# Optimization experiments

Measured on AMD Instinct MI355X. Metric: run time of the kernel, lower is better.

## Reference

```python
import jax, jax.numpy as jnp
import numpy as np

N = 50000          # nodes
E = 400000         # edges
F = 128            # num_embeddings
NUM_TYPES = 100    # num_atoms (embedding vocab)
CUTOFF = 5.0
N_RBF = 20


def _silu(x):
    return x * jax.nn.sigmoid(x)


def setup_inputs() -> dict:
    key = jax.random.key(0)
    ks = jax.random.split(key, 16)
    pos = jax.random.normal(ks[0], (N, 3), dtype=jnp.float32) * 3.0
    z = jax.random.randint(ks[1], (N,), 0, NUM_TYPES)
    dst = jax.random.randint(ks[2], (E,), 0, N)
    # ensure src != dst so distances are nonzero
    src = (dst + 1 + jax.random.randint(ks[3], (E,), 0, N - 1)) % N
    def lin(k, fan_in, fan_out):
        kw, kb = jax.random.split(k)
        lim = 1.0 / np.sqrt(fan_in)
        W = jax.random.uniform(kw, (fan_out, fan_in), minval=-lim, maxval=lim, dtype=jnp.float32)
        b = jax.random.uniform(kb, (fan_out,), minval=-lim, maxval=lim, dtype=jnp.float32)
        return W, b
    emb_table = jax.random.normal(ks[4], (NUM_TYPES, F), dtype=jnp.float32)
    Wp1, bp1 = lin(ks[5], F, F)
    Wp2, bp2 = lin(ks[6], F, 3 * F)
    Ww, bw = lin(ks[7], N_RBF, 3 * F)
    Wu, bu = lin(ks[8], F, F)
    Wv, bv = lin(ks[9], F, F)
    Wu1, bu1 = lin(ks[10], 2 * F, F)
    Wu2, bu2 = lin(ks[11], F, 3 * F)
    return dict(pos=pos, emb_table=emb_table,
                Wp1=Wp1, bp1=bp1, Wp2=Wp2, bp2=bp2, Ww=Ww, bw=bw,
                Wu=Wu, bu=bu, Wv=Wv, bv=bv, Wu1=Wu1, bu1=bu1, Wu2=Wu2, bu2=bu2,
                z=z, src=src, dst=dst)


def painn_forward(pos, emb_table, Wp1, bp1, Wp2, bp2, Ww, bw, Wu, bu, Wv, bv,
                  Wu1, bu1, Wu2, bu2, z, src, dst):
    s = emb_table[z]                                  # [N,F] scalar features
    v = jnp.zeros((N, F, 3), dtype=s.dtype)          # equivariant features

    # ---- message block ----
    phi = _silu(s @ Wp1.T + bp1) @ Wp2.T + bp2       # [N,3F]
    rel = pos[dst] - pos[src]                        # [E,3]
    d = jnp.maximum(jnp.linalg.norm(rel, axis=-1), 1e-9)  # [E]
    n = jnp.arange(1, N_RBF + 1, dtype=jnp.float32)
    rbf = jnp.sin(n * jnp.pi * d[:, None] / CUTOFF) / d[:, None]   # [E,20]
    Wf = rbf @ Ww.T + bw                             # [E,3F]
    split = phi[src] * Wf                            # [E,3F] gated message
    ds = jax.ops.segment_sum(split[:, :F], dst, num_segments=N)    # [N,F]
    direction = rel / d[:, None]                     # [E,3]
    dv_e = v[src] * split[:, F:2 * F, None] + split[:, 2 * F:, None] * direction[:, None, :]  # [E,F,3]
    dv = jax.ops.segment_sum(dv_e, dst, num_segments=N)            # [N,F,3]
    s = s + ds
    v = v + dv

    # ---- update block ----
    U = jnp.einsum('nfc,gf->ngc', v, Wu) + bu[:, None]   # [N,F,3]
    V = jnp.einsum('nfc,gf->ngc', v, Wv) + bv[:, None]   # [N,F,3]
    Vn = jnp.linalg.norm(V, axis=-1)                     # [N,F]
    h = jnp.concatenate([s, Vn], axis=-1)                # [N,2F]
    a = _silu(h @ Wu1.T + bu1) @ Wu2.T + bu2             # [N,3F]
    dv2 = U * a[:, :F, None]                             # [N,F,3]
    ds2 = a[:, F:2 * F] + jnp.sum(U * V, axis=-1) * a[:, 2 * F:]   # [N,F]
    return s + ds2, v + dv2


def reference(pos, emb_table, Wp1, bp1, Wp2, bp2, Ww, bw, Wu, bu, Wv, bv,
              Wu1, bu1, Wu2, bu2, z, src, dst):
    return painn_forward(pos, emb_table, Wp1, bp1, Wp2, bp2, Ww, bw, Wu, bu,
                         Wv, bv, Wu1, bu1, Wu2, bu2, z, src, dst)
```

## Files before the change

### kernel.cpp

```cpp
#include <hip/hip_runtime.h>

#define NN 50000
#define EE 400000
#define FF 128
#define NRBF 20
#define MAXDEG 64
#define PI_OVER_CUT 0.6283185307179586f

typedef _Float16 h8 __attribute__((ext_vector_type(8)));
typedef float    f4 __attribute__((ext_vector_type(4)));

union pk32 { unsigned int u; _Float16 h[2]; };

__global__ __launch_bounds__(256) void k_bucket(const int* __restrict__ dst,
                                                int* __restrict__ counts,
                                                int* __restrict__ slots) {
    int e = blockIdx.x * 256 + threadIdx.x;
    if (e < EE) {
        int n = dst[e];
        int slot = atomicAdd(&counts[n], 1);
        if (slot < MAXDEG) slots[n * MAXDEG + slot] = e;
    }
}

__global__ __launch_bounds__(256) void k_wconv(
    const float* __restrict__ Wu, const float* __restrict__ Wv,
    const float* __restrict__ Wu1, const float* __restrict__ Wu2,
    const float* __restrict__ Wp1, const float* __restrict__ Wp2,
    const float* __restrict__ Ww, const float* __restrict__ bw,
    _Float16* __restrict__ Wuh, _Float16* __restrict__ Wvh,
    _Float16* __restrict__ Wu1h, _Float16* __restrict__ Wu2h,
    _Float16* __restrict__ Wp1h, _Float16* __restrict__ Wp2h,
    _Float16* __restrict__ Wwh32, int* __restrict__ counts)
{
    int i = blockIdx.x * 256 + threadIdx.x;
    if (i < NN) counts[i] = 0;
    if (i < 16384) { Wuh[i] = (_Float16)Wu[i]; Wvh[i] = (_Float16)Wv[i];
                     Wp1h[i] = (_Float16)Wp1[i]; }
    if (i < 32768) { Wu1h[i] = (_Float16)Wu1[i]; }
    if (i < 49152) { Wu2h[i] = (_Float16)Wu2[i]; Wp2h[i] = (_Float16)Wp2[i]; }
    if (i < 8192) {
        int col = i >> 5, k = i & 31;
        int sr = col < 128 ? col : col + 128;
        _Float16 v = (_Float16)0.f;
        if (k < 20)       v = (_Float16)Ww[sr * NRBF + k];
        else if (k == 20) v = (_Float16)bw[sr];
        Wwh32[i] = v;
    }
}

__global__ __launch_bounds__(256) void k_node_phi_mfma(
    const float* __restrict__ emb, const int* __restrict__ z,
    const _Float16* __restrict__ Wp1h, const float* __restrict__ bp1,
    const _Float16* __restrict__ Wp2h, const float* __restrict__ bp2,
    unsigned int* __restrict__ phi_pk, _Float16* __restrict__ s_h)
{
    __shared__ _Float16 Ss[32 * 128];
    __shared__ _Float16 H1s[32 * 128];

    const int t    = threadIdx.x;
    const int lane = t & 63;
    const int w    = t >> 6;
    const int lr   = lane & 15;
    const int lq   = lane >> 4;
    const int n0   = blockIdx.x * 32;
    const f4 z4 = {0.f, 0.f, 0.f, 0.f};

    for (int i = t; i < 512; i += 256) {
        int n = i >> 4, gr = i & 15;
        int nn = n0 + n; if (nn > NN - 1) nn = NN - 1;
        const float* sp = &emb[(size_t)z[nn] * FF + gr * 8];
        float4 aa = *(const float4*)sp;
        float4 bb = *(const float4*)(sp + 4);
        h8 hv;
        hv[0] = (_Float16)aa.x; hv[1] = (_Float16)aa.y;
        hv[2] = (_Float16)aa.z; hv[3] = (_Float16)aa.w;
        hv[4] = (_Float16)bb.x; hv[5] = (_Float16)bb.y;
        hv[6] = (_Float16)bb.z; hv[7] = (_Float16)bb.w;
        *(h8*)&Ss[(n * 16 + (gr ^ (n & 15))) * 8] = hv;
        *(h8*)&s_h[(size_t)nn * FF + gr * 8] = hv;
    }
    __syncthreads();

    f4 acc1[2][2];
    #pragma unroll
    for (int a = 0; a < 2; ++a)
        #pragma unroll
        for (int m = 0; m < 2; ++m) acc1[a][m] = z4;
    {
        const _Float16* bb = Wp1h + (size_t)lr * 128 + lq * 8;
        #pragma unroll
        for (int g2 = 0; g2 < 2; ++g2) {
            h8 bf[4];
            #pragma unroll
            for (int ks = 0; ks < 4; ++ks)
                bf[ks] = *(const h8*)(bb + ((2 * w + g2) * 16) * 128 + ks * 32);
            #pragma unroll
            for (int mt = 0; mt < 2; ++mt) {
                const int r = mt * 16 + lr;
                #pragma unroll
                for (int ks = 0; ks < 4; ++ks) {
                    h8 af = *(const h8*)&Ss[(r * 16 + ((ks * 4 + lq) ^ (r & 15))) * 8];
                    acc1[g2][mt] = __builtin_amdgcn_mfma_f32_16x16x32_f16(
                        af, bf[ks], acc1[g2][mt], 0, 0, 0);
                }
            }
        }
    }
    #pragma unroll
    for (int g2 = 0; g2 < 2; ++g2) {
        const int g = (2 * w + g2) * 16 + lr;
        const float b1 = bp1[g];
        #pragma unroll
        for (int mt = 0; mt < 2; ++mt)
            #pragma unroll
            for (int r = 0; r < 4; ++r) {
                float x = acc1[g2][mt][r] + b1;
                float y = x / (1.f + __expf(-x));
                int n = mt * 16 + lq * 4 + r;
                H1s[(n * 16 + ((g >> 3) ^ (n & 15))) * 8 + (g & 7)] = (_Float16)y;
            }
    }
    __syncthreads();

    f4 accS[2][2], accV[2][2];
    #pragma unroll
    for (int a = 0; a < 2; ++a)
        #pragma unroll
        for (int m = 0; m < 2; ++m) { accS[a][m] = z4; accV[a][m] = z4; }
    {
        const _Float16* bbs = Wp2h + (size_t)lr * 128 + lq * 8;
        const _Float16* bbv = Wp2h + (size_t)(256 + lr) * 128 + lq * 8;
        #pragma unroll
        for (int g2 = 0; g2 < 2; ++g2) {
            h8 bfs[4], bfv[4];
            #pragma unroll
            for (int ks = 0; ks < 4; ++ks) {
                bfs[ks] = *(const h8*)(bbs + ((2 * w + g2) * 16) * 128 + ks * 32);
                bfv[ks] = *(const h8*)(bbv + ((2 * w + g2) * 16) * 128 + ks * 32);
            }
            #pragma unroll
            for (int mt = 0; mt < 2; ++mt) {
                const int r = mt * 16 + lr;
                #pragma unroll
                for (int ks = 0; ks < 4; ++ks) {
                    h8 af = *(const h8*)&H1s[(r * 16 + ((ks * 4 + lq) ^ (r & 15))) * 8];
                    accS[g2][mt] = __builtin_amdgcn_mfma_f32_16x16x32_f16(
                        af, bfs[ks], accS[g2][mt], 0, 0, 0);
                    accV[g2][mt] = __builtin_amdgcn_mfma_f32_16x16x32_f16(
                        af, bfv[ks], accV[g2][mt], 0, 0, 0);
                }
            }
        }
    }
    #pragma unroll
    for (int g2 = 0; g2 < 2; ++g2) {
        const int g = (2 * w + g2) * 16 + lr;
        const float bsa = bp2[g], bva = bp2[256 + g];
        #pragma unroll
        for (int mt = 0; mt < 2; ++mt)
            #pragma unroll
            for (int r = 0; r < 4; ++r) {
                int n = mt * 16 + lq * 4 + r;
                int nn = n0 + n;
                if (nn < NN) {
                    pk32 pk;
                    pk.h[0] = (_Float16)(accS[g2][mt][r] + bsa);
                    pk.h[1] = (_Float16)(accV[g2][mt][r] + bva);
                    phi_pk[(size_t)nn * FF + g] = pk.u;
                }
            }
    }
}

__global__ __launch_bounds__(128) void k_edge_mfma(
    const float* __restrict__ pos,
    const _Float16* __restrict__ Wwh32,
    const int* __restrict__ src,
    const int* __restrict__ counts, const int* __restrict__ slots,
    const unsigned int* __restrict__ phi_pk,
    _Float16* __restrict__ s_h,
    _Float16* __restrict__ xg)
{
    __shared__ _Float16 A[16 * 32];
    __shared__ float dirs[16][4];
    __shared__ unsigned int wf[16 * 130];

    const int t    = threadIdx.x;
    const int lane = t & 63;
    const int w    = t >> 6;
    const int lr   = lane & 15;
    const int lq   = lane >> 4;
    const int n    = blockIdx.x;
    const int m    = t & 15;
    const int kk   = t >> 4;
    const f4 z4 = {0.f, 0.f, 0.f, 0.f};

    h8 bf[8];
    #pragma unroll
    for (int j = 0; j < 8; ++j)
        bf[j] = *(const h8*)&Wwh32[(size_t)((w * 8 + j) * 16 + lr) * 32 + lq * 8];

    const float px = pos[3 * n], py = pos[3 * n + 1], pz = pos[3 * n + 2];

    int deg = counts[n];
    deg = deg > MAXDEG ? MAXDEG : deg;

    const size_t gi = (size_t)n * FF + t;
    float s_old = (float)s_h[gi];

    float acc_s = 0.f, av0 = 0.f, av1 = 0.f, av2 = 0.f;

    for (int t0 = 0; t0 < deg; t0 += 16) {
        const int degT = (deg - t0) < 16 ? (deg - t0) : 16;
        __syncthreads();
        {
            int mc = (m < degT) ? m : 0;
            int e  = slots[n * MAXDEG + t0 + mc];
            int sI = src[e];
            float rx = px - pos[3 * sI];
            float ry = py - pos[3 * sI + 1];
            float rz = pz - pos[3 * sI + 2];
            float d = sqrtf(rx * rx + ry * ry + rz * rz);
            d = fmaxf(d, 1e-9f);
            float di = 1.f / d;
            if (t < 16) {
                dirs[t][0] = rx * di;
                dirs[t][1] = ry * di;
                dirs[t][2] = rz * di;
                dirs[t][3] = __int_as_float(sI);
            }
            float v0 = __sinf((float)(kk + 1) * PI_OVER_CUT * d) * di;
            float v1 = __sinf((float)(kk + 9) * PI_OVER_CUT * d) * di;
            float v2;
            if (kk < 4)       v2 = __sinf((float)(kk + 17) * PI_OVER_CUT * d) * di;
            else if (kk == 4) v2 = 1.0f;
            else              v2 = 0.f;
            #define STO(K, V) A[m * 32 + (((K) >> 3) ^ (m & 3)) * 8 + ((K) & 7)] = (_Float16)(V)
            STO(kk,      v0);
            STO(kk + 8,  v1);
            STO(kk + 16, v2);
            STO(kk + 24, 0.f);
            #undef STO
        }
        __syncthreads();
        {
            h8 af = *(const h8*)&A[(lr * 4 + (lq ^ (lr & 3))) * 8];
            #pragma unroll
            for (int j = 0; j < 8; ++j) {
                f4 dd = __builtin_amdgcn_mfma_f32_16x16x32_f16(af, bf[j], z4, 0, 0, 0);
                #pragma unroll
                for (int r = 0; r < 4; ++r) {
                    int mm = lq * 4 + r;
                    ((_Float16*)&wf[mm * 130 + j * 16 + lr])[w] = (_Float16)dd[r];
                }
            }
        }
        __syncthreads();
        {
            unsigned int phr[16];
            #pragma unroll
            for (int mm = 0; mm < 16; ++mm) {
                int sim = __float_as_int(dirs[mm][3]);
                phr[mm] = (mm < degT) ? phi_pk[(size_t)sim * FF + t] : 0u;
            }
            #pragma unroll
            for (int mm = 0; mm < 16; ++mm) {
                if (mm < degT) {
                    pk32 ph, wfu;
                    ph.u  = phr[mm];
                    wfu.u = wf[mm * 130 + t];
                    float ps = (float)ph.h[0] * (float)wfu.h[0];
                    float pv = (float)ph.h[1] * (float)wfu.h[1];
                    acc_s += ps;
                    av0 = fmaf(pv, dirs[mm][0], av0);
                    av1 = fmaf(pv, dirs[mm][1], av1);
                    av2 = fmaf(pv, dirs[mm][2], av2);
                }
            }
        }
    }

    s_h[gi] = (_Float16)(s_old + acc_s);
    xg[((size_t)n * 3 + 0) * FF + t] = (_Float16)av0;
    xg[((size_t)n * 3 + 1) * FF + t] = (_Float16)av1;
    xg[((size_t)n * 3 + 2) * FF + t] = (_Float16)av2;
}

__global__ __launch_bounds__(256) void k_update_mfma(
    const _Float16* __restrict__ xg, const _Float16* __restrict__ s_h,
    const _Float16* __restrict__ Wuh, const _Float16* __restrict__ Wvh,
    const _Float16* __restrict__ Wu1h, const _Float16* __restrict__ Wu2h,
    const float* __restrict__ bu, const float* __restrict__ bv,
    const float* __restrict__ bu1, const float* __restrict__ bu2,
    float* __restrict__ s_io, float* __restrict__ v_io)
{
    __shared__ _Float16 Xs[48 * 128];
    __shared__ _Float16 Hs[16 * 256];
    __shared__ _Float16 H1s[16 * 128];

    const int t    = threadIdx.x;
    const int lane = t & 63;
    const int w    = t >> 6;
    const int lr   = lane & 15;
    const int lq   = lane >> 4;
    const int n0   = blockIdx.x * 16;
    const f4 z4 = {0.f, 0.f, 0.f, 0.f};

    for (int i = t; i < 768; i += 256) {
        int row = i >> 4, gr = i & 15;
        int n = row & 15, c = row >> 4;
        int nn = n0 + n; if (nn > NN - 1) nn = NN - 1;
        uint4 d = *(const uint4*)&xg[((size_t)nn * 3 + c) * FF + gr * 8];
        *(uint4*)&Xs[(row * 16 + (gr ^ n)) * 8] = d;
    }
    {
        int n = t >> 4, gr = t & 15;
        int nn = n0 + n; if (nn > NN - 1) nn = NN - 1;
        uint4 d = *(const uint4*)&s_h[(size_t)nn * FF + gr * 8];
        *(uint4*)&Hs[(n * 32 + (gr ^ n)) * 8] = d;
    }
    __syncthreads();

    f4 accU[2][3], accV[2][3];
    #pragma unroll
    for (int a = 0; a < 2; ++a)
        #pragma unroll
        for (int c = 0; c < 3; ++c) { accU[a][c] = z4; accV[a][c] = z4; }

    {
        const _Float16* bb = Wuh + (size_t)lr * 128 + lq * 8;
        h8 bfr[2][4];
        #pragma unroll
        for (int g2 = 0; g2 < 2; ++g2)
            #pragma unroll
            for (int ks = 0; ks < 4; ++ks)
                bfr[g2][ks] = *(const h8*)(bb + ((2 * w + g2) * 16) * 128 + ks * 32);
        #pragma unroll
        for (int c = 0; c < 3; ++c) {
            const int rr = c * 16 + lr;
            h8 af[4];
            #pragma unroll
            for (int ks = 0; ks < 4; ++ks)
                af[ks] = *(const h8*)&Xs[(rr * 16 + ((ks * 4 + lq) ^ lr)) * 8];
            #pragma unroll
            for (int g2 = 0; g2 < 2; ++g2)
                #pragma unroll
                for (int ks = 0; ks < 4; ++ks)
                    accU[g2][c] = __builtin_amdgcn_mfma_f32_16x16x32_f16(
                        af[ks], bfr[g2][ks], accU[g2][c], 0, 0, 0);
        }
    }
    {
        const _Float16* bb = Wvh + (size_t)lr * 128 + lq * 8;
        h8 bfr[2][4];
        #pragma unroll
        for (int g2 = 0; g2 < 2; ++g2)
            #pragma unroll
            for (int ks = 0; ks < 4; ++ks)
                bfr[g2][ks] = *(const h8*)(bb + ((2 * w + g2) * 16) * 128 + ks * 32);
        #pragma unroll
        for (int c = 0; c < 3; ++c) {
            const int rr = c * 16 + lr;
            h8 af[4];
            #pragma unroll
            for (int ks = 0; ks < 4; ++ks)
                af[ks] = *(const h8*)&Xs[(rr * 16 + ((ks * 4 + lq) ^ lr)) * 8];
            #pragma unroll
            for (int g2 = 0; g2 < 2; ++g2)
                #pragma unroll
                for (int ks = 0; ks < 4; ++ks)
                    accV[g2][c] = __builtin_amdgcn_mfma_f32_16x16x32_f16(
                        af[ks], bfr[g2][ks], accV[g2][c], 0, 0, 0);
        }
    }

    float uvr[2][4];
    #pragma unroll
    for (int g2 = 0; g2 < 2; ++g2) {
        const int g = (2 * w + g2) * 16 + lr;
        const float bU = bu[g], bV = bv[g];
        #pragma unroll
        for (int r = 0; r < 4; ++r) {
            float Ux = accU[g2][0][r] + bU;
            float Uy = accU[g2][1][r] + bU;
            float Uz = accU[g2][2][r] + bU;
            float Vx = accV[g2][0][r] + bV;
            float Vy = accV[g2][1][r] + bV;
            float Vz = accV[g2][2][r] + bV;
            accU[g2][0][r] = Ux;
            accU[g2][1][r] = Uy;
            accU[g2][2][r] = Uz;
            uvr[g2][r] = Ux * Vx + Uy * Vy + Uz * Vz;
            float vn = sqrtf(Vx * Vx + Vy * Vy + Vz * Vz);
            int n = lq * 4 + r;
            int gr = 16 + (g >> 3);
            Hs[(n * 32 + (gr ^ n)) * 8 + (g & 7)] = (_Float16)vn;
        }
    }
    __syncthreads();

    f4 acc2[2];
    acc2[0] = z4; acc2[1] = z4;
    {
        const _Float16* bb = Wu1h + (size_t)lr * 256 + lq * 8;
        #pragma unroll
        for (int g2 = 0; g2 < 2; ++g2) {
            h8 bfr[8];
            #pragma unroll
            for (int ks = 0; ks < 8; ++ks)
                bfr[ks] = *(const h8*)(bb + ((2 * w + g2) * 16) * 256 + ks * 32);
            #pragma unroll
            for (int ks = 0; ks < 8; ++ks) {
                h8 af = *(const h8*)&Hs[(lr * 32 + ((ks * 4 + lq) ^ lr)) * 8];
                acc2[g2] = __builtin_amdgcn_mfma_f32_16x16x32_f16(
                    af, bfr[ks], acc2[g2], 0, 0, 0);
            }
        }
    }
    #pragma unroll
    for (int g2 = 0; g2 < 2; ++g2) {
        const int g = (2 * w + g2) * 16 + lr;
        const float b1 = bu1[g];
        #pragma unroll
        for (int r = 0; r < 4; ++r) {
            float x = acc2[g2][r] + b1;
            float y = x / (1.f + __expf(-x));
            int n = lq * 4 + r;
            H1s[(n * 16 + ((g >> 3) ^ n)) * 8 + (g & 7)] = (_Float16)y;
        }
    }
    __syncthreads();

    f4 acc3[3][2];
    #pragma unroll
    for (int a = 0; a < 3; ++a) { acc3[a][0] = z4; acc3[a][1] = z4; }
    {
        const _Float16* bb = Wu2h + (size_t)lr * 128 + lq * 8;
        #pragma unroll
        for (int ai = 0; ai < 3; ++ai)
            #pragma unroll
            for (int g2 = 0; g2 < 2; ++g2) {
                const int jt = ai * 8 + 2 * w + g2;
                h8 bfr[4];
                #pragma unroll
                for (int ks = 0; ks < 4; ++ks)
                    bfr[ks] = *(const h8*)(bb + (size_t)(jt * 16) * 128 + ks * 32);
                #pragma unroll
                for (int ks = 0; ks < 4; ++ks) {
                    h8 af = *(const h8*)&H1s[(lr * 16 + ((ks * 4 + lq) ^ lr)) * 8];
                    acc3[ai][g2] = __builtin_amdgcn_mfma_f32_16x16x32_f16(
                        af, bfr[ks], acc3[ai][g2], 0, 0, 0);
                }
            }
    }

    #pragma unroll
    for (int g2 = 0; g2 < 2; ++g2) {
        const int g = (2 * w + g2) * 16 + lr;
        const float b1 = bu2[g], b2 = bu2[128 + g], b3 = bu2[256 + g];
        #pragma unroll
        for (int r = 0; r < 4; ++r) {
            int n = lq * 4 + r;
            int nn = n0 + n;
            if (nn < NN) {
                float a1 = acc3[0][g2][r] + b1;
                float a2 = acc3[1][g2][r] + b2;
                float a3 = acc3[2][g2][r] + b3;
                size_t gi = (size_t)nn * FF + g;
                float s1 = (float)Hs[(n * 32 + ((g >> 3) ^ n)) * 8 + (g & 7)];
                s_io[gi] = s1 + a2 + uvr[g2][r] * a3;
                float vx = (float)Xs[((0 * 16 + n) * 16 + ((g >> 3) ^ n)) * 8 + (g & 7)];
                float vy = (float)Xs[((1 * 16 + n) * 16 + ((g >> 3) ^ n)) * 8 + (g & 7)];
                float vz = (float)Xs[((2 * 16 + n) * 16 + ((g >> 3) ^ n)) * 8 + (g & 7)];
                v_io[gi * 3 + 0] = vx + accU[g2][0][r] * a1;
                v_io[gi * 3 + 1] = vy + accU[g2][1][r] * a1;
                v_io[gi * 3 + 2] = vz + accU[g2][2][r] * a1;
            }
        }
    }
}

extern "C" void kernel_launch(void* const* d_in, const int* in_sizes, int n_in,
                              void* d_out, int out_size, void* d_ws, size_t ws_size,
                              hipStream_t stream)
{
    const float* pos = (const float*)d_in[0];
    const float* emb = (const float*)d_in[1];
    const float* Wp1 = (const float*)d_in[2];
    const float* bp1 = (const float*)d_in[3];
    const float* Wp2 = (const float*)d_in[4];
    const float* bp2 = (const float*)d_in[5];
    const float* Ww  = (const float*)d_in[6];
    const float* bw  = (const float*)d_in[7];
    const float* Wu  = (const float*)d_in[8];
    const float* bu  = (const float*)d_in[9];
    const float* Wv  = (const float*)d_in[10];
    const float* bv  = (const float*)d_in[11];
    const float* Wu1 = (const float*)d_in[12];
    const float* bu1 = (const float*)d_in[13];
    const float* Wu2 = (const float*)d_in[14];
    const float* bu2 = (const float*)d_in[15];
    const int* z   = (const int*)d_in[16];
    const int* src = (const int*)d_in[17];
    const int* dst = (const int*)d_in[18];

    float* s_io = (float*)d_out;
    float* v_io = (float*)d_out + (size_t)NN * FF;

    char* ws = (char*)d_ws;
    unsigned int* phi_pk = (unsigned int*)ws;
    _Float16* xg    = (_Float16*)(phi_pk + (size_t)NN * FF);
    _Float16* s_h   = xg + (size_t)NN * 3 * FF;
    _Float16* Wuh   = s_h + (size_t)NN * FF;
    _Float16* Wvh   = Wuh  + 128 * 128;
    _Float16* Wu1h  = Wvh  + 128 * 128;
    _Float16* Wu2h  = Wu1h + 128 * 256;
    _Float16* Wp1h  = Wu2h + 384 * 128;
    _Float16* Wp2h  = Wp1h + 128 * 128;
    _Float16* Wwh32 = Wp2h + 384 * 128;
    int* counts = (int*)(Wwh32 + 256 * 32);
    int* slots  = counts + NN;

    k_wconv <<<196, 256, 0, stream>>>(Wu, Wv, Wu1, Wu2, Wp1, Wp2, Ww, bw,
                                      Wuh, Wvh, Wu1h, Wu2h, Wp1h, Wp2h, Wwh32,
                                      counts);
    k_bucket<<<(EE + 255) / 256, 256, 0, stream>>>(dst, counts, slots);
    k_node_phi_mfma<<<(NN + 31) / 32, 256, 0, stream>>>(emb, z, Wp1h, bp1,
                                                        Wp2h, bp2,
                                                        phi_pk, s_h);
    k_edge_mfma<<<NN, 128, 0, stream>>>(pos, Wwh32, src, counts, slots,
                                        phi_pk, s_h, xg);
    k_update_mfma<<<(NN + 15) / 16, 256, 0, stream>>>(xg, s_h,
                                                      Wuh, Wvh, Wu1h, Wu2h,
                                                      bu, bv, bu1, bu2,
                                                      s_io, v_io);
}
```

Baseline: 382.2 us.

## Make edge kernel waves independent to remove block-wide barriers

Each of the two waves in the edge kernel now handles its own 64 features end to end. Each wave recomputes the RBF tile, runs the MFMAs for its own scalar and vector filter columns, and keeps private shared-memory buffers. This removes all three __syncthreads per 16-edge tile and reads the source index with readfirstlane so the phi gather address is uniform across the wave. The cost is that the sin/RBF and geometry work is duplicated across both waves. The code also relies on lockstep execution within a wave for the shared-memory handoffs, since no barriers remain.

```diff
diff --git a/kernel.cpp b/kernel.cpp
--- a/kernel.cpp
+++ b/kernel.cpp
@@ -182,38 +182,41 @@
     _Float16* __restrict__ s_h,
     _Float16* __restrict__ xg)
 {
-    __shared__ _Float16 A[16 * 32];
-    __shared__ float dirs[16][4];
-    __shared__ unsigned int wf[16 * 130];
+    __shared__ _Float16 A[2][16 * 32];
+    __shared__ float dirs[2][16][4];
+    __shared__ unsigned int wfi[2][16 * 66];
 
     const int t    = threadIdx.x;
     const int lane = t & 63;
     const int w    = t >> 6;
     const int lr   = lane & 15;
     const int lq   = lane >> 4;
+    const int m    = lane & 15;
+    const int ks   = lane >> 4;
     const int n    = blockIdx.x;
-    const int m    = t & 15;
-    const int kk   = t >> 4;
     const f4 z4 = {0.f, 0.f, 0.f, 0.f};
 
     h8 bf[8];
     #pragma unroll
-    for (int j = 0; j < 8; ++j)
-        bf[j] = *(const h8*)&Wwh32[(size_t)((w * 8 + j) * 16 + lr) * 32 + lq * 8];
+    for (int js = 0; js < 8; ++js) {
+        int col = (js < 4) ? (w * 64 + js * 16 + lr)
+                           : (128 + w * 64 + (js - 4) * 16 + lr);
+        bf[js] = *(const h8*)&Wwh32[(size_t)col * 32 + lq * 8];
+    }
 
     const float px = pos[3 * n], py = pos[3 * n + 1], pz = pos[3 * n + 2];
 
     int deg = counts[n];
     deg = deg > MAXDEG ? MAXDEG : deg;
 
-    const size_t gi = (size_t)n * FF + t;
+    const int gf = w * 64 + lane;
+    const size_t gi = (size_t)n * FF + gf;
     float s_old = (float)s_h[gi];
 
     float acc_s = 0.f, av0 = 0.f, av1 = 0.f, av2 = 0.f;
 
     for (int t0 = 0; t0 < deg; t0 += 16) {
         const int degT = (deg - t0) < 16 ? (deg - t0) : 16;
-        __syncthreads();
         {
             int mc = (m < degT) ? m : 0;
             int e  = slots[n * MAXDEG + t0 + mc];
@@ -224,67 +227,68 @@
             float d = sqrtf(rx * rx + ry * ry + rz * rz);
             d = fmaxf(d, 1e-9f);
             float di = 1.f / d;
-            if (t < 16) {
-                dirs[t][0] = rx * di;
-                dirs[t][1] = ry * di;
-                dirs[t][2] = rz * di;
-                dirs[t][3] = __int_as_float(sI);
-            }
-            float v0 = __sinf((float)(kk + 1) * PI_OVER_CUT * d) * di;
-            float v1 = __sinf((float)(kk + 9) * PI_OVER_CUT * d) * di;
-            float v2;
-            if (kk < 4)       v2 = __sinf((float)(kk + 17) * PI_OVER_CUT * d) * di;
-            else if (kk == 4) v2 = 1.0f;
-            else              v2 = 0.f;
-            #define STO(K, V) A[m * 32 + (((K) >> 3) ^ (m & 3)) * 8 + ((K) & 7)] = (_Float16)(V)
-            STO(kk,      v0);
-            STO(kk + 8,  v1);
-            STO(kk + 16, v2);
-            STO(kk + 24, 0.f);
-            #undef STO
-        }
-        __syncthreads();
+            if (lane < 16) {
+                dirs[w][lane][0] = rx * di;
+                dirs[w][lane][1] = ry * di;
+                dirs[w][lane][2] = rz * di;
+                dirs[w][lane][3] = __int_as_float(sI);
+            }
+            float vv[8];
+            #pragma unroll
+            for (int j = 0; j < 5; ++j)
+                vv[j] = __sinf((float)(ks + 4 * j + 1) * PI_OVER_CUT * d) * di;
+            vv[5] = (ks == 0) ? 1.0f : 0.f;
+            vv[6] = 0.f; vv[7] = 0.f;
+            #pragma unroll
+            for (int j = 0; j < 8; ++j) {
+                int k = ks + 4 * j;
+                A[w][m * 32 + (((k >> 3) ^ (m & 3)) * 8) + (k & 7)] = (_Float16)vv[j];
+            }
+        }
         {
-            h8 af = *(const h8*)&A[(lr * 4 + (lq ^ (lr & 3))) * 8];
-            #pragma unroll
-            for (int j = 0; j < 8; ++j) {
-                f4 dd = __builtin_amdgcn_mfma_f32_16x16x32_f16(af, bf[j], z4, 0, 0, 0);
+            h8 af = *(const h8*)&A[w][(lr * 4 + (lq ^ (lr & 3))) * 8];
+            #pragma unroll
+            for (int js = 0; js < 4; ++js) {
+                f4 dd_s = __builtin_amdgcn_mfma_f32_16x16x32_f16(af, bf[js],     z4, 0, 0, 0);
+                f4 dd_v = __builtin_amdgcn_mfma_f32_16x16x32_f16(af, bf[js + 4], z4, 0, 0, 0);
                 #pragma unroll
                 for (int r = 0; r < 4; ++r) {
-                    int mm = lq * 4 + r;
-                    ((_Float16*)&wf[mm * 130 + j * 16 + lr])[w] = (_Float16)dd[r];
+                    pk32 pk;
+                    pk.h[0] = (_Float16)dd_s[r];
+                    pk.h[1] = (_Float16)dd_v[r];
+                    wfi[w][(lq * 4 + r) * 66 + js * 16 + lr] = pk.u;
                 }
             }
         }
-        __syncthreads();
         {
             unsigned int phr[16];
             #pragma unroll
             for (int mm = 0; mm < 16; ++mm) {
-                int sim = __float_as_int(dirs[mm][3]);
-                phr[mm] = (mm < degT) ? phi_pk[(size_t)sim * FF + t] : 0u;
+                int sim = __builtin_amdgcn_readfirstlane(
+                              __float_as_int(dirs[w][mm][3]));
+                phr[mm] = (mm < degT) ? phi_pk[(size_t)sim * FF + gf] : 0u;
             }
             #pragma unroll
             for (int mm = 0; mm < 16; ++mm) {
                 if (mm < degT) {
                     pk32 ph, wfu;
                     ph.u  = phr[mm];
-                    wfu.u = wf[mm * 130 + t];
+                    wfu.u = wfi[w][mm * 66 + lane];
                     float ps = (float)ph.h[0] * (float)wfu.h[0];
                     float pv = (float)ph.h[1] * (float)wfu.h[1];
                     acc_s += ps;
-                    av0 = fmaf(pv, dirs[mm][0], av0);
-                    av1 = fmaf(pv, dirs[mm][1], av1);
-                    av2 = fmaf(pv, dirs[mm][2], av2);
+                    av0 = fmaf(pv, dirs[w][mm][0], av0);
+                    av1 = fmaf(pv, dirs[w][mm][1], av1);
+                    av2 = fmaf(pv, dirs[w][mm][2], av2);
                 }
             }
         }
     }
 
     s_h[gi] = (_Float16)(s_old + acc_s);
-    xg[((size_t)n * 3 + 0) * FF + t] = (_Float16)av0;
-    xg[((size_t)n * 3 + 1) * FF + t] = (_Float16)av1;
-    xg[((size_t)n * 3 + 2) * FF + t] = (_Float16)av2;
+    xg[((size_t)n * 3 + 0) * FF + gf] = (_Float16)av0;
+    xg[((size_t)n * 3 + 1) * FF + gf] = (_Float16)av1;
+    xg[((size_t)n * 3 + 2) * FF + gf] = (_Float16)av2;
 }
 
 __global__ __launch_bounds__(256) void k_update_mfma(
```

Result: no change. 379.3 us (-0.7%).
